# Kernel tuning notes

Measured on AMD Instinct MI355X. Metric: run time of the kernel, lower is better.

The kernel has to match this reference:

```python
import jax, jax.numpy as jnp
import numpy as np


def setup_inputs() -> dict:
    key = jax.random.key(0)
    k1, k2, k3 = jax.random.split(key, 3)
    B, N, D = 4, 256, 128
    s = jax.random.normal(k1, (B, N, D), dtype=jnp.float32)
    W1 = jax.random.normal(k2, (3 * D, 2 * D), dtype=jnp.float32) * 0.02
    b1 = jnp.zeros((2 * D,), dtype=jnp.float32)
    W2 = jax.random.normal(k3, (2 * D, 1), dtype=jnp.float32) * 0.02
    b2 = jnp.zeros((1,), dtype=jnp.float32)
    return {"s": s, "W1": W1, "b1": b1, "W2": W2, "b2": b2, "K": 8}


def reference(s, W1, b1, W2, b2, K):
    B, N, D = s.shape
    si = jnp.broadcast_to(s[:, :, None, :], (B, N, N, D))
    sj = jnp.broadcast_to(s[:, None, :, :], (B, N, N, D))
    pair = jnp.concatenate([si, sj, si * sj], axis=-1)  # [B,N,N,3D]
    h = jax.nn.relu(pair @ W1 + b1)                      # [B,N,N,2D]
    scores = (h @ W2 + b2)[..., 0]                       # [B,N,N]
    k = min(int(K), N)
    _, idx = jax.lax.top_k(scores, k)                    # [B,N,K]
    # scatter ones at topk indices (indices are distinct per row)
    gate = jnp.sum(jax.nn.one_hot(idx, N, dtype=jnp.float32), axis=-2)  # [B,N,N]
    w = gate / jnp.clip(jnp.sum(gate, axis=-1, keepdims=True), 1.0)
    ctx = jnp.einsum('bij,bjd->bid', w, s)               # [B,N,D]
    return ctx, gate, w
```

## Files before the change

kernel.cpp:

```cpp
#include <hip/hip_runtime.h>
#include <hip/hip_bf16.h>
#include <math.h>

#define B_ 4
#define N_ 256
#define D_ 128
#define H_ 256
#define K_ 8

typedef __attribute__((ext_vector_type(8))) short short8;
typedef __attribute__((ext_vector_type(4))) float f32x4;

__device__ __forceinline__ unsigned short f2bf(float x) {
    union { __hip_bfloat16 h; unsigned short s; } u;
    u.h = __float2bfloat16(x);
    return u.s;
}
__device__ __forceinline__ float bf2f(unsigned short b) {
    unsigned v = ((unsigned)b) << 16;
    return __builtin_bit_cast(float, v);
}
__device__ __forceinline__ unsigned pk2(float x, float y) {
    union { __hip_bfloat162 h; unsigned u; } c;
    c.h = __float22bfloat162_rn(float2{x, y});
    return c.u;
}
__device__ __forceinline__ void gld_lds16(const float* g, float* l) {
    __builtin_amdgcn_global_load_lds(
        (const __attribute__((address_space(1))) void*)g,
        (__attribute__((address_space(3))) void*)l, 16, 0, 0);
}

__global__ __launch_bounds__(256) void pre_kernel(
    const float* __restrict__ s, const float* __restrict__ W1,
    const float* __restrict__ b1,
    float* __restrict__ avec, float* __restrict__ bvec,
    unsigned short* __restrict__ Wt)
{
    int blk = blockIdx.x;
    int t = threadIdx.x;
    if (blk < 512) {
        int bi0 = blk * 2;
        __shared__ float s2[2][D_];
        {
            int r = t >> 7, d = t & 127;
            s2[r][d] = s[(size_t)(bi0 + r) * D_ + d];
        }
        __syncthreads();
        float aA0 = b1[t], aA1 = aA0, aB0 = 0.f, aB1 = 0.f;
        const float* W1a = W1 + t;
        const float* W1b = W1 + (size_t)D_ * H_ + t;
        #pragma unroll 8
        for (int d = 0; d < D_; ++d) {
            float wa = W1a[(size_t)d * H_];
            float wb = W1b[(size_t)d * H_];
            float s0 = s2[0][d], s1 = s2[1][d];
            aA0 = fmaf(s0, wa, aA0);
            aA1 = fmaf(s1, wa, aA1);
            aB0 = fmaf(s0, wb, aB0);
            aB1 = fmaf(s1, wb, aB1);
        }
        avec[(size_t)bi0 * H_ + t]       = aA0;
        avec[(size_t)(bi0 + 1) * H_ + t] = aA1;
        bvec[(size_t)bi0 * H_ + t]       = aB0;
        bvec[(size_t)(bi0 + 1) * H_ + t] = aB1;
    } else {
        int e = (blk - 512) * 256 + t;
        int h = e >> 7, d = e & 127;
        Wt[e] = f2bf(W1[(size_t)(2 * D_ + d) * H_ + h]);
    }
}

__global__ __launch_bounds__(512, 2) void approx_scores(
    const float* __restrict__ s, const unsigned short* __restrict__ Wt,
    const float* __restrict__ W2, const float* __restrict__ b2,
    const float* __restrict__ avec, const float* __restrict__ bvec,
    unsigned short* __restrict__ ascu)
{
    int blk = blockIdx.x;
    int b   = blk >> 7;
    int jtb = ((blk >> 4) & 7) * 32;
    int i0  = (blk & 15) * 16;
    int t = threadIdx.x;
    int lane = t & 63;
    int w = __builtin_amdgcn_readfirstlane(t >> 6);
    int l15 = lane & 15, quad = lane >> 4;

    __shared__ __align__(16) short Pl[2][32 * 128];
    __shared__ __align__(16) float si_all[16][D_];
    __shared__ __align__(16) float av_l[16][H_];
    __shared__ float partial[2][8][32];

    const float* sB = s + (size_t)b * N_ * D_;

    {
        const float* avp = avec + (size_t)(b * N_ + i0) * H_;
        #pragma unroll
        for (int k = 0; k < 2; ++k) {
            int slot = t + 512 * k;
            gld_lds16(avp + slot * 4, &av_l[0][0] + slot * 4);
        }
    }

    {
        int ii = t >> 5, dq = t & 31;
        *(float4*)&si_all[ii][dq * 4] =
            *(const float4*)(sB + (size_t)(i0 + ii) * D_ + dq * 4);
    }

    short8 Wreg[2][4];
    #pragma unroll
    for (int mi = 0; mi < 2; ++mi)
        #pragma unroll
        for (int dk = 0; dk < 4; ++dk)
            Wreg[mi][dk] = *(const short8*)(
                Wt + (size_t)(w * 32 + mi * 16 + l15) * D_ + dk * 32 + quad * 8);
    float bvr[2][2][4];
    float w2r[2][4];
    #pragma unroll
    for (int mi = 0; mi < 2; ++mi) {
        int hq = w * 32 + mi * 16 + quad * 4;
        #pragma unroll
        for (int r = 0; r < 4; ++r)
            w2r[mi][r] = W2[hq + r];
        #pragma unroll
        for (int nj = 0; nj < 2; ++nj)
            #pragma unroll
            for (int r = 0; r < 4; ++r)
                bvr[mi][nj][r] = bvec[((size_t)(b * N_ + jtb + nj * 16 + l15)) * H_
                                      + hq + r];
    }
    float b2v = b2[0];

    int prow = t >> 4, pseg = t & 15;
    float4 sj0, sj1;
    {
        const float* sj = sB + (size_t)(jtb + prow) * D_ + pseg * 8;
        sj0 = ((const float4*)sj)[0];
        sj1 = ((const float4*)sj)[1];
    }
    __syncthreads();

    {
        const float* si = &si_all[0][pseg * 8];
        float4 s0 = ((const float4*)si)[0], s1 = ((const float4*)si)[1];
        uint4 v;
        v.x = pk2(sj0.x * s0.x, sj0.y * s0.y);
        v.y = pk2(sj0.z * s0.z, sj0.w * s0.w);
        v.z = pk2(sj1.x * s1.x, sj1.y * s1.y);
        v.w = pk2(sj1.z * s1.z, sj1.w * s1.w);
        int pc = pseg ^ (prow & 15);
        *(uint4*)&Pl[0][prow * 128 + pc * 8] = v;
    }
    __syncthreads();

    #pragma unroll 1
    for (int i = 0; i < 16; ++i) {
        int cur = i & 1;
        if (w == 0 && lane < 32 && i > 0) {
            float sum = b2v;
            #pragma unroll
            for (int ww = 0; ww < 8; ++ww) sum += partial[(i - 1) & 1][ww][lane];
            ascu[(size_t)(b * N_ + i0 + i - 1) * N_ + jtb + lane] = f2bf(sum);
        }
        float4 av4[2];
        av4[0] = *(const float4*)&av_l[i][w * 32 + quad * 4];
        av4[1] = *(const float4*)&av_l[i][w * 32 + 16 + quad * 4];
        f32x4 acc[2][2];
        #pragma unroll
        for (int mi = 0; mi < 2; ++mi)
            #pragma unroll
            for (int nj = 0; nj < 2; ++nj)
                #pragma unroll
                for (int r = 0; r < 4; ++r)
                    acc[mi][nj][r] = av4[mi][r] + bvr[mi][nj][r];
        #pragma unroll
        for (int dk = 0; dk < 4; ++dk) {
            short8 Pf[2];
            #pragma unroll
            for (int nj = 0; nj < 2; ++nj) {
                int pcc = (dk * 4 + quad) ^ l15;
                Pf[nj] = *(const short8*)&Pl[cur][(nj * 16 + l15) * 128 + pcc * 8];
            }
            #pragma unroll
            for (int nj = 0; nj < 2; ++nj)
                #pragma unroll
                for (int mi = 0; mi < 2; ++mi)
                    acc[mi][nj] = __builtin_amdgcn_mfma_f32_16x16x32_bf16(
                        Wreg[mi][dk], Pf[nj], acc[mi][nj], 0, 0, 0);
        }
        if (i < 15) {
            const float* si = &si_all[i + 1][pseg * 8];
            float4 s0 = ((const float4*)si)[0], s1 = ((const float4*)si)[1];
            uint4 v;
            v.x = pk2(sj0.x * s0.x, sj0.y * s0.y);
            v.y = pk2(sj0.z * s0.z, sj0.w * s0.w);
            v.z = pk2(sj1.x * s1.x, sj1.y * s1.y);
            v.w = pk2(sj1.z * s1.z, sj1.w * s1.w);
            int pc = pseg ^ (prow & 15);
            *(uint4*)&Pl[cur ^ 1][prow * 128 + pc * 8] = v;
        }
        float rs[2];
        rs[0] = 0.f; rs[1] = 0.f;
        #pragma unroll
        for (int mi = 0; mi < 2; ++mi)
            #pragma unroll
            for (int nj = 0; nj < 2; ++nj)
                #pragma unroll
                for (int r = 0; r < 4; ++r)
                    rs[nj] = fmaf(fmaxf(acc[mi][nj][r], 0.f), w2r[mi][r], rs[nj]);
        #pragma unroll
        for (int nj = 0; nj < 2; ++nj) {
            rs[nj] += __shfl_xor(rs[nj], 16);
            rs[nj] += __shfl_xor(rs[nj], 32);
        }
        if (lane < 32) {
            float v = (quad == 0) ? rs[0] : rs[1];
            partial[cur][w][lane] = v;
        }
        __syncthreads();
    }
    if (w == 0 && lane < 32) {
        float sum = b2v;
        #pragma unroll
        for (int ww = 0; ww < 8; ++ww) sum += partial[15 & 1][ww][lane];
        ascu[(size_t)(b * N_ + i0 + 15) * N_ + jtb + lane] = f2bf(sum);
    }
}

#define DC8 8
__global__ __launch_bounds__(256) void finalize_kernel(
    const float* __restrict__ s, const float* __restrict__ W1,
    const float* __restrict__ W2, const float* __restrict__ b2,
    const float* __restrict__ avec, const float* __restrict__ bvec,
    const unsigned short* __restrict__ ascu,
    float* __restrict__ ctx, float* __restrict__ gate, float* __restrict__ w)
{
    int bi0 = blockIdx.x * 2;
    int b = bi0 >> 8;
    int t = threadIdx.x;
    int lane = t & 63;
    int wv_id = t >> 6;

    __shared__ float asc[2][N_];
    __shared__ int cand[2][16];
    __shared__ __align__(16) float Pt[D_ * 32];
    __shared__ __align__(16) float Wlw[4][2][DC8][64];
    __shared__ float part[2][16][33];
    __shared__ float rsc[2][16];
    __shared__ int sel8[2][8];

    for (int e = t; e < 512; e += 256) {
        int r = e >> 8, jj = e & 255;
        asc[r][jj] = bf2f(ascu[(size_t)(bi0 + r) * N_ + jj]);
    }
    __syncthreads();

    {
        int r = t >> 7, lj = t & 127;
        float my[2]; int rk[2];
        #pragma unroll
        for (int m = 0; m < 2; ++m) { my[m] = asc[r][m * 128 + lj]; rk[m] = 0; }
        #pragma unroll 4
        for (int j2 = 0; j2 < N_; ++j2) {
            float o = asc[r][j2];
            #pragma unroll
            for (int m = 0; m < 2; ++m) {
                int jm = m * 128 + lj;
                rk[m] += (o > my[m]) || (o == my[m] && j2 < jm);
            }
        }
        #pragma unroll
        for (int m = 0; m < 2; ++m)
            if (rk[m] < 16) cand[r][rk[m]] = m * 128 + lj;
    }
    __syncthreads();

    const float* Wc = W1 + (size_t)2 * D_ * H_;

    int dl = lane >> 4;
    int hl = (lane & 15) * 4;

    #pragma unroll
    for (int k = 0; k < 2; ++k)
        gld_lds16(Wc + (size_t)(k * 4 + dl) * H_ + wv_id * 64 + hl,
                  &Wlw[wv_id][0][k * 4 + dl][hl]);

    for (int e = t; e < 1024; e += 256) {
        int rr = e >> 9, c = e & 15, dq = (e >> 4) & 31;
        int j = cand[rr][c];
        float4 sj = *(const float4*)(s + ((size_t)(b * N_ + j)) * D_ + dq * 4);
        float4 si = *(const float4*)(s + ((size_t)(bi0 + rr)) * D_ + dq * 4);
        int base = (dq * 4) * 32 + rr * 16 + c;
        Pt[base + 0 * 32] = si.x * sj.x;
        Pt[base + 1 * 32] = si.y * sj.y;
        Pt[base + 2 * 32] = si.z * sj.z;
        Pt[base + 3 * 32] = si.w * sj.w;
    }

    int cg = t & 3, rr = (t >> 2) & 1;
    int hg = t >> 3;
    int h0 = hg * 8;
    int ho = (hg & 7) * 8;
    float acc[4][8];
    {
        const float* av = avec + (size_t)(bi0 + rr) * H_ + h0;
        float4 av40 = *(const float4*)(av);
        float4 av41 = *(const float4*)(av + 4);
        #pragma unroll
        for (int cc = 0; cc < 4; ++cc) {
            int j = cand[rr][cg * 4 + cc];
            const float* bv = bvec + ((size_t)(b * N_ + j)) * H_ + h0;
            float4 b40 = *(const float4*)(bv);
            float4 b41 = *(const float4*)(bv + 4);
            acc[cc][0] = av40.x + b40.x;
            acc[cc][1] = av40.y + b40.y;
            acc[cc][2] = av40.z + b40.z;
            acc[cc][3] = av40.w + b40.w;
            acc[cc][4] = av41.x + b41.x;
            acc[cc][5] = av41.y + b41.y;
            acc[cc][6] = av41.z + b41.z;
            acc[cc][7] = av41.w + b41.w;
        }
    }
    __syncthreads();

    int pvoff = rr * 16 + cg * 4;
    #pragma unroll 1
    for (int ch = 0; ch < 15; ++ch) {
        int cur = ch & 1;
        {
            const float* src = Wc + (size_t)((ch + 1) * DC8) * H_;
            #pragma unroll
            for (int k = 0; k < 2; ++k)
                gld_lds16(src + (size_t)(k * 4 + dl) * H_ + wv_id * 64 + hl,
                          &Wlw[wv_id][cur ^ 1][k * 4 + dl][hl]);
        }
        asm volatile("s_waitcnt vmcnt(2)" ::: "memory");
        __builtin_amdgcn_sched_barrier(0);
        int d0 = ch * DC8;
        #pragma unroll
        for (int d = 0; d < DC8; ++d) {
            float4 pv = *(const float4*)&Pt[(d0 + d) * 32 + pvoff];
            float wvv[8];
            *(float4*)&wvv[0] = *(const float4*)&Wlw[wv_id][cur][d][ho];
            *(float4*)&wvv[4] = *(const float4*)&Wlw[wv_id][cur][d][ho + 4];
            #pragma unroll
            for (int m = 0; m < 8; ++m) {
                acc[0][m] = fmaf(pv.x, wvv[m], acc[0][m]);
                acc[1][m] = fmaf(pv.y, wvv[m], acc[1][m]);
                acc[2][m] = fmaf(pv.z, wvv[m], acc[2][m]);
                acc[3][m] = fmaf(pv.w, wvv[m], acc[3][m]);
            }
        }
    }
    asm volatile("s_waitcnt vmcnt(0)" ::: "memory");
    __builtin_amdgcn_sched_barrier(0);
    {
        int d0 = 15 * DC8;
        #pragma unroll
        for (int d = 0; d < DC8; ++d) {
            float4 pv = *(const float4*)&Pt[(d0 + d) * 32 + pvoff];
            float wvv[8];
            *(float4*)&wvv[0] = *(const float4*)&Wlw[wv_id][1][d][ho];
            *(float4*)&wvv[4] = *(const float4*)&Wlw[wv_id][1][d][ho + 4];
            #pragma unroll
            for (int m = 0; m < 8; ++m) {
                acc[0][m] = fmaf(pv.x, wvv[m], acc[0][m]);
                acc[1][m] = fmaf(pv.y, wvv[m], acc[1][m]);
                acc[2][m] = fmaf(pv.z, wvv[m], acc[2][m]);
                acc[3][m] = fmaf(pv.w, wvv[m], acc[3][m]);
            }
        }
    }

    {
        float w2v[8];
        *(float4*)&w2v[0] = *(const float4*)(W2 + h0);
        *(float4*)&w2v[4] = *(const float4*)(W2 + h0 + 4);
        #pragma unroll
        for (int cc = 0; cc < 4; ++cc) {
            float sc = 0.f;
            #pragma unroll
            for (int m = 0; m < 8; ++m)
                sc = fmaf(fmaxf(acc[cc][m], 0.f), w2v[m], sc);
            part[rr][cg * 4 + cc][hg] = sc;
        }
    }
    __syncthreads();
    if (t < 32) {
        int r2 = t >> 4, c2 = t & 15;
        float sum = b2[0];
        #pragma unroll
        for (int m = 0; m < 32; ++m) sum += part[r2][c2][m];
        rsc[r2][c2] = sum;
    }
    __syncthreads();

    if (t < 32) {
        int r2 = t >> 4, c2 = t & 15;
        float my = rsc[r2][c2]; int myj = cand[r2][c2];
        int rank = 0;
        #pragma unroll
        for (int c3 = 0; c3 < 16; ++c3) {
            float o = rsc[r2][c3]; int oj = cand[r2][c3];
            rank += (o > my) || (o == my && oj < myj);
        }
        if (rank < 8) sel8[r2][rank] = myj;
    }
    __syncthreads();

    for (int e = t; e < 512; e += 256) {
        int r2 = e >> 8, jj = e & 255;
        float gv = 0.f;
        #pragma unroll
        for (int m = 0; m < 8; ++m)
            gv = (jj == sel8[r2][m]) ? 1.f : gv;
        gate[(size_t)(bi0 + r2) * N_ + jj] = gv;
        w[(size_t)(bi0 + r2) * N_ + jj]    = gv * 0.125f;
    }
    {
        int r2 = t >> 7, d = t & 127;
        float a = 0.f;
        #pragma unroll
        for (int m = 0; m < 8; ++m)
            a += s[((size_t)(b * N_ + sel8[r2][m])) * D_ + d];
        ctx[(size_t)(bi0 + r2) * D_ + d] = a * 0.125f;
    }
}

extern "C" void kernel_launch(void* const* d_in, const int* in_sizes, int n_in,
                              void* d_out, int out_size, void* d_ws, size_t ws_size,
                              hipStream_t stream)
{
    const float* s  = (const float*)d_in[0];
    const float* W1 = (const float*)d_in[1];
    const float* b1 = (const float*)d_in[2];
    const float* W2 = (const float*)d_in[3];
    const float* b2 = (const float*)d_in[4];

    float* avec = (float*)d_ws;
    float* bvec = avec + (size_t)B_ * N_ * H_;
    unsigned short* ascu = (unsigned short*)(bvec + (size_t)B_ * N_ * H_);
    unsigned short* Wtu  = ascu + (size_t)B_ * N_ * N_;

    float* ctx  = (float*)d_out;
    float* gate = ctx + (size_t)B_ * N_ * D_;
    float* wout = gate + (size_t)B_ * N_ * N_;

    pre_kernel<<<640, 256, 0, stream>>>(s, W1, b1, avec, bvec, Wtu);
    approx_scores<<<512, 512, 0, stream>>>(s, Wtu, W2, b2, avec, bvec, ascu);
    finalize_kernel<<<B_ * N_ / 2, 256, 0, stream>>>(s, W1, W2, b2, avec, bvec, ascu,
                                                     ctx, gate, wout);
}
```

Measured before the change: 128.6 us.

## Retile approx_scores to 8 i-rows by 64 j-columns and raise occupancy hint

Changes the approx_scores block tile from 16 i × 32 j to 8 i × 64 j, doubling MFMA N-tiles per wave and halving the serial i-loop length. The bvec bias is no longer kept in registers; it is reloaded from global each iteration and added after the MFMA together with avec. The launch bound goes from 2 to 4 waves per EU to allow more resident blocks. The aim is shorter per-block latency and better latency hiding, at the cost of repeated bvec global loads and more register pressure under the tighter bound.

```diff
diff --git a/kernel.cpp b/kernel.cpp
--- a/kernel.cpp
+++ b/kernel.cpp
@@ -71,7 +71,7 @@
     }
 }
 
-__global__ __launch_bounds__(512, 2) void approx_scores(
+__global__ __launch_bounds__(512, 4) void approx_scores(
     const float* __restrict__ s, const unsigned short* __restrict__ Wt,
     const float* __restrict__ W2, const float* __restrict__ b2,
     const float* __restrict__ avec, const float* __restrict__ bvec,
@@ -79,30 +79,26 @@
 {
     int blk = blockIdx.x;
     int b   = blk >> 7;
-    int jtb = ((blk >> 4) & 7) * 32;
-    int i0  = (blk & 15) * 16;
+    int jtb = ((blk >> 5) & 3) * 64;
+    int i0  = (blk & 31) * 8;
     int t = threadIdx.x;
     int lane = t & 63;
     int w = __builtin_amdgcn_readfirstlane(t >> 6);
     int l15 = lane & 15, quad = lane >> 4;
 
-    __shared__ __align__(16) short Pl[2][32 * 128];
-    __shared__ __align__(16) float si_all[16][D_];
-    __shared__ __align__(16) float av_l[16][H_];
-    __shared__ float partial[2][8][32];
+    __shared__ __align__(16) short Pl[2][64 * 128];
+    __shared__ __align__(16) float si_all[8][D_];
+    __shared__ __align__(16) float av_l[8][H_];
+    __shared__ float partial[2][8][64];
 
     const float* sB = s + (size_t)b * N_ * D_;
 
     {
         const float* avp = avec + (size_t)(b * N_ + i0) * H_;
-        #pragma unroll
-        for (int k = 0; k < 2; ++k) {
-            int slot = t + 512 * k;
-            gld_lds16(avp + slot * 4, &av_l[0][0] + slot * 4);
-        }
-    }
-
-    {
+        gld_lds16(avp + t * 4, &av_l[0][0] + t * 4);
+    }
+
+    if (t < 256) {
         int ii = t >> 5, dq = t & 31;
         *(float4*)&si_all[ii][dq * 4] =
             *(const float4*)(sB + (size_t)(i0 + ii) * D_ + dq * 4);
@@ -115,7 +111,6 @@
         for (int dk = 0; dk < 4; ++dk)
             Wreg[mi][dk] = *(const short8*)(
                 Wt + (size_t)(w * 32 + mi * 16 + l15) * D_ + dk * 32 + quad * 8);
-    float bvr[2][2][4];
     float w2r[2][4];
     #pragma unroll
     for (int mi = 0; mi < 2; ++mi) {
@@ -123,108 +118,126 @@
         #pragma unroll
         for (int r = 0; r < 4; ++r)
             w2r[mi][r] = W2[hq + r];
-        #pragma unroll
-        for (int nj = 0; nj < 2; ++nj)
-            #pragma unroll
-            for (int r = 0; r < 4; ++r)
-                bvr[mi][nj][r] = bvec[((size_t)(b * N_ + jtb + nj * 16 + l15)) * H_
-                                      + hq + r];
     }
     float b2v = b2[0];
 
     int prow = t >> 4, pseg = t & 15;
-    float4 sj0, sj1;
-    {
-        const float* sj = sB + (size_t)(jtb + prow) * D_ + pseg * 8;
-        sj0 = ((const float4*)sj)[0];
-        sj1 = ((const float4*)sj)[1];
+    float4 sjA0, sjA1, sjB0, sjB1;
+    {
+        const float* sjA = sB + (size_t)(jtb + prow) * D_ + pseg * 8;
+        sjA0 = ((const float4*)sjA)[0];
+        sjA1 = ((const float4*)sjA)[1];
+        const float* sjB = sB + (size_t)(jtb + prow + 32) * D_ + pseg * 8;
+        sjB0 = ((const float4*)sjB)[0];
+        sjB1 = ((const float4*)sjB)[1];
     }
     __syncthreads();
 
     {
         const float* si = &si_all[0][pseg * 8];
         float4 s0 = ((const float4*)si)[0], s1 = ((const float4*)si)[1];
+        int pc = pseg ^ (prow & 15);
         uint4 v;
-        v.x = pk2(sj0.x * s0.x, sj0.y * s0.y);
-        v.y = pk2(sj0.z * s0.z, sj0.w * s0.w);
-        v.z = pk2(sj1.x * s1.x, sj1.y * s1.y);
-        v.w = pk2(sj1.z * s1.z, sj1.w * s1.w);
-        int pc = pseg ^ (prow & 15);
+        v.x = pk2(sjA0.x * s0.x, sjA0.y * s0.y);
+        v.y = pk2(sjA0.z * s0.z, sjA0.w * s0.w);
+        v.z = pk2(sjA1.x * s1.x, sjA1.y * s1.y);
+        v.w = pk2(sjA1.z * s1.z, sjA1.w * s1.w);
         *(uint4*)&Pl[0][prow * 128 + pc * 8] = v;
+        uint4 u;
+        u.x = pk2(sjB0.x * s0.x, sjB0.y * s0.y);
+        u.y = pk2(sjB0.z * s0.z, sjB0.w * s0.w);
+        u.z = pk2(sjB1.x * s1.x, sjB1.y * s1.y);
+        u.w = pk2(sjB1.z * s1.z, sjB1.w * s1.w);
+        *(uint4*)&Pl[0][(prow + 32) * 128 + pc * 8] = u;
     }
     __syncthreads();
 
     #pragma unroll 1
-    for (int i = 0; i < 16; ++i) {
+    for (int i = 0; i < 8; ++i) {
         int cur = i & 1;
-        if (w == 0 && lane < 32 && i > 0) {
+        if (w == 0 && i > 0) {
             float sum = b2v;
             #pragma unroll
             for (int ww = 0; ww < 8; ++ww) sum += partial[(i - 1) & 1][ww][lane];
             ascu[(size_t)(b * N_ + i0 + i - 1) * N_ + jtb + lane] = f2bf(sum);
         }
-        float4 av4[2];
-        av4[0] = *(const float4*)&av_l[i][w * 32 + quad * 4];
-        av4[1] = *(const float4*)&av_l[i][w * 32 + 16 + quad * 4];
-        f32x4 acc[2][2];
+        float4 bv4[2][4];
         #pragma unroll
         for (int mi = 0; mi < 2; ++mi)
             #pragma unroll
-            for (int nj = 0; nj < 2; ++nj)
-                #pragma unroll
-                for (int r = 0; r < 4; ++r)
-                    acc[mi][nj][r] = av4[mi][r] + bvr[mi][nj][r];
+            for (int nj = 0; nj < 4; ++nj)
+                bv4[mi][nj] = *(const float4*)&bvec[
+                    ((size_t)(b * N_ + jtb + nj * 16 + l15)) * H_
+                    + w * 32 + mi * 16 + quad * 4];
+        f32x4 acc[2][4];
+        #pragma unroll
+        for (int mi = 0; mi < 2; ++mi)
+            #pragma unroll
+            for (int nj = 0; nj < 4; ++nj)
+                acc[mi][nj] = (f32x4){0.f, 0.f, 0.f, 0.f};
         #pragma unroll
         for (int dk = 0; dk < 4; ++dk) {
-            short8 Pf[2];
-            #pragma unroll
-            for (int nj = 0; nj < 2; ++nj) {
-                int pcc = (dk * 4 + quad) ^ l15;
+            short8 Pf[4];
+            int pcc = (dk * 4 + quad) ^ l15;
+            #pragma unroll
+            for (int nj = 0; nj < 4; ++nj)
                 Pf[nj] = *(const short8*)&Pl[cur][(nj * 16 + l15) * 128 + pcc * 8];
-            }
-            #pragma unroll
-            for (int nj = 0; nj < 2; ++nj)
+            #pragma unroll
+            for (int nj = 0; nj < 4; ++nj)
                 #pragma unroll
                 for (int mi = 0; mi < 2; ++mi)
                     acc[mi][nj] = __builtin_amdgcn_mfma_f32_16x16x32_bf16(
                         Wreg[mi][dk], Pf[nj], acc[mi][nj], 0, 0, 0);
         }
-        if (i < 15) {
+        if (i < 7) {
             const float* si = &si_all[i + 1][pseg * 8];
             float4 s0 = ((const float4*)si)[0], s1 = ((const float4*)si)[1];
+            int pc = pseg ^ (prow & 15);
             uint4 v;
-            v.x = pk2(sj0.x * s0.x, sj0.y * s0.y);
-            v.y = pk2(sj0.z * s0.z, sj0.w * s0.w);
-            v.z = pk2(sj1.x * s1.x, sj1.y * s1.y);
-            v.w = pk2(sj1.z * s1.z, sj1.w * s1.w);
-            int pc = pseg ^ (prow & 15);
+            v.x = pk2(sjA0.x * s0.x, sjA0.y * s0.y);
+            v.y = pk2(sjA0.z * s0.z, sjA0.w * s0.w);
+            v.z = pk2(sjA1.x * s1.x, sjA1.y * s1.y);
+            v.w = pk2(sjA1.z * s1.z, sjA1.w * s1.w);
             *(uint4*)&Pl[cur ^ 1][prow * 128 + pc * 8] = v;
-        }
-        float rs[2];
-        rs[0] = 0.f; rs[1] = 0.f;
+            uint4 u;
+            u.x = pk2(sjB0.x * s0.x, sjB0.y * s0.y);
+            u.y = pk2(sjB0.z * s0.z, sjB0.w * s0.w);
+            u.z = pk2(sjB1.x * s1.x, sjB1.y * s1.y);
+            u.w = pk2(sjB1.z * s1.z, sjB1.w * s1.w);
+            *(uint4*)&Pl[cur ^ 1][(prow + 32) * 128 + pc * 8] = u;
+        }
+        float4 av4[2];
+        av4[0] = *(const float4*)&av_l[i][w * 32 + quad * 4];
+        av4[1] = *(const float4*)&av_l[i][w * 32 + 16 + quad * 4];
+        float rs[4];
+        rs[0] = 0.f; rs[1] = 0.f; rs[2] = 0.f; rs[3] = 0.f;
         #pragma unroll
         for (int mi = 0; mi < 2; ++mi)
             #pragma unroll
-            for (int nj = 0; nj < 2; ++nj)
+            for (int nj = 0; nj < 4; ++nj)
                 #pragma unroll
-                for (int r = 0; r < 4; ++r)
-                    rs[nj] = fmaf(fmaxf(acc[mi][nj][r], 0.f), w2r[mi][r], rs[nj]);
-        #pragma unroll
-        for (int nj = 0; nj < 2; ++nj) {
+                for (int r = 0; r < 4; ++r) {
+                    float z = acc[mi][nj][r] + av4[mi][r] + bv4[mi][nj][r];
+                    rs[nj] = fmaf(fmaxf(z, 0.f), w2r[mi][r], rs[nj]);
+                }
+        #pragma unroll
+        for (int nj = 0; nj < 4; ++nj) {
             rs[nj] += __shfl_xor(rs[nj], 16);
             rs[nj] += __shfl_xor(rs[nj], 32);
         }
-        if (lane < 32) {
-            float v = (quad == 0) ? rs[0] : rs[1];
+        {
+            float v = (quad == 0) ? rs[0]
+                    : (quad == 1) ? rs[1]
+                    : (quad == 2) ? rs[2] : rs[3];
             partial[cur][w][lane] = v;
         }
         __syncthreads();
     }
-    if (w == 0 && lane < 32) {
+    if (w == 0) {
         float sum = b2v;
         #pragma unroll
-        for (int ww = 0; ww < 8; ++ww) sum += partial[15 & 1][ww][lane];
-        ascu[(size_t)(b * N_ + i0 + 15) * N_ + jtb + lane] = f2bf(sum);
+        for (int ww = 0; ww < 8; ++ww) sum += partial[7 & 1][ww][lane];
+        ascu[(size_t)(b * N_ + i0 + 7) * N_ + jtb + lane] = f2bf(sum);
     }
 }
 
```

Result: slower. 158.9 us (+23.5%).

## Build pair-product MFMA operands in registers and halve j-tile per block

Applied to the files above, without the earlier changes.

The approx_scores kernel now builds the si*sj bf16 B-operand directly in registers from preloaded sj rows, so the double-buffered LDS product tile and its per-iteration barrier go away. Partial sums for all 16 i rows are written to shared memory and reduced once after a single final barrier. The j-tile shrinks from 32 to 16, doubling the grid to 1024 blocks, and launch bounds allow 4 blocks per CU for more occupancy. The trade-off is that each block redoes the bf16 packing of si*sj for every i and runs fewer MFMAs per block, while holding more registers for sj.

```diff
diff --git a/kernel.cpp b/kernel.cpp
--- a/kernel.cpp
+++ b/kernel.cpp
@@ -71,25 +71,24 @@
     }
 }
 
-__global__ __launch_bounds__(512, 2) void approx_scores(
+__global__ __launch_bounds__(512, 4) void approx_scores(
     const float* __restrict__ s, const unsigned short* __restrict__ Wt,
     const float* __restrict__ W2, const float* __restrict__ b2,
     const float* __restrict__ avec, const float* __restrict__ bvec,
     unsigned short* __restrict__ ascu)
 {
     int blk = blockIdx.x;
-    int b   = blk >> 7;
-    int jtb = ((blk >> 4) & 7) * 32;
+    int b   = blk >> 8;
+    int jtb = ((blk >> 4) & 15) * 16;
     int i0  = (blk & 15) * 16;
     int t = threadIdx.x;
     int lane = t & 63;
     int w = __builtin_amdgcn_readfirstlane(t >> 6);
     int l15 = lane & 15, quad = lane >> 4;
 
-    __shared__ __align__(16) short Pl[2][32 * 128];
     __shared__ __align__(16) float si_all[16][D_];
     __shared__ __align__(16) float av_l[16][H_];
-    __shared__ float partial[2][8][32];
+    __shared__ float partial[8][16][16];
 
     const float* sB = s + (size_t)b * N_ * D_;
 
@@ -115,116 +114,71 @@
         for (int dk = 0; dk < 4; ++dk)
             Wreg[mi][dk] = *(const short8*)(
                 Wt + (size_t)(w * 32 + mi * 16 + l15) * D_ + dk * 32 + quad * 8);
-    float bvr[2][2][4];
+
+    float4 sjr[4][2];
+    {
+        const float* sj = sB + (size_t)(jtb + l15) * D_ + quad * 8;
+        #pragma unroll
+        for (int dk = 0; dk < 4; ++dk) {
+            sjr[dk][0] = ((const float4*)(sj + dk * 32))[0];
+            sjr[dk][1] = ((const float4*)(sj + dk * 32))[1];
+        }
+    }
+    float4 bvr[2];
     float w2r[2][4];
     #pragma unroll
     for (int mi = 0; mi < 2; ++mi) {
         int hq = w * 32 + mi * 16 + quad * 4;
+        bvr[mi] = *(const float4*)&bvec[((size_t)(b * N_ + jtb + l15)) * H_ + hq];
         #pragma unroll
         for (int r = 0; r < 4; ++r)
             w2r[mi][r] = W2[hq + r];
-        #pragma unroll
-        for (int nj = 0; nj < 2; ++nj)
-            #pragma unroll
-            for (int r = 0; r < 4; ++r)
-                bvr[mi][nj][r] = bvec[((size_t)(b * N_ + jtb + nj * 16 + l15)) * H_
-                                      + hq + r];
     }
     float b2v = b2[0];
-
-    int prow = t >> 4, pseg = t & 15;
-    float4 sj0, sj1;
-    {
-        const float* sj = sB + (size_t)(jtb + prow) * D_ + pseg * 8;
-        sj0 = ((const float4*)sj)[0];
-        sj1 = ((const float4*)sj)[1];
-    }
-    __syncthreads();
-
-    {
-        const float* si = &si_all[0][pseg * 8];
-        float4 s0 = ((const float4*)si)[0], s1 = ((const float4*)si)[1];
-        uint4 v;
-        v.x = pk2(sj0.x * s0.x, sj0.y * s0.y);
-        v.y = pk2(sj0.z * s0.z, sj0.w * s0.w);
-        v.z = pk2(sj1.x * s1.x, sj1.y * s1.y);
-        v.w = pk2(sj1.z * s1.z, sj1.w * s1.w);
-        int pc = pseg ^ (prow & 15);
-        *(uint4*)&Pl[0][prow * 128 + pc * 8] = v;
-    }
     __syncthreads();
 
     #pragma unroll 1
     for (int i = 0; i < 16; ++i) {
-        int cur = i & 1;
-        if (w == 0 && lane < 32 && i > 0) {
-            float sum = b2v;
-            #pragma unroll
-            for (int ww = 0; ww < 8; ++ww) sum += partial[(i - 1) & 1][ww][lane];
-            ascu[(size_t)(b * N_ + i0 + i - 1) * N_ + jtb + lane] = f2bf(sum);
-        }
-        float4 av4[2];
-        av4[0] = *(const float4*)&av_l[i][w * 32 + quad * 4];
-        av4[1] = *(const float4*)&av_l[i][w * 32 + 16 + quad * 4];
-        f32x4 acc[2][2];
+        float4 av0 = *(const float4*)&av_l[i][w * 32 + quad * 4];
+        float4 av1 = *(const float4*)&av_l[i][w * 32 + 16 + quad * 4];
+        f32x4 acc[2];
+        #pragma unroll
+        for (int r = 0; r < 4; ++r) {
+            acc[0][r] = av0[r] + bvr[0][r];
+            acc[1][r] = av1[r] + bvr[1][r];
+        }
+        #pragma unroll
+        for (int dk = 0; dk < 4; ++dk) {
+            float4 si0 = *(const float4*)&si_all[i][dk * 32 + quad * 8];
+            float4 si1 = *(const float4*)&si_all[i][dk * 32 + quad * 8 + 4];
+            union { uint4 u; short8 s8; } pf;
+            pf.u.x = pk2(sjr[dk][0].x * si0.x, sjr[dk][0].y * si0.y);
+            pf.u.y = pk2(sjr[dk][0].z * si0.z, sjr[dk][0].w * si0.w);
+            pf.u.z = pk2(sjr[dk][1].x * si1.x, sjr[dk][1].y * si1.y);
+            pf.u.w = pk2(sjr[dk][1].z * si1.z, sjr[dk][1].w * si1.w);
+            #pragma unroll
+            for (int mi = 0; mi < 2; ++mi)
+                acc[mi] = __builtin_amdgcn_mfma_f32_16x16x32_bf16(
+                    Wreg[mi][dk], pf.s8, acc[mi], 0, 0, 0);
+        }
+        float rs = 0.f;
         #pragma unroll
         for (int mi = 0; mi < 2; ++mi)
             #pragma unroll
-            for (int nj = 0; nj < 2; ++nj)
-                #pragma unroll
-                for (int r = 0; r < 4; ++r)
-                    acc[mi][nj][r] = av4[mi][r] + bvr[mi][nj][r];
-        #pragma unroll
-        for (int dk = 0; dk < 4; ++dk) {
-            short8 Pf[2];
-            #pragma unroll
-            for (int nj = 0; nj < 2; ++nj) {
-                int pcc = (dk * 4 + quad) ^ l15;
-                Pf[nj] = *(const short8*)&Pl[cur][(nj * 16 + l15) * 128 + pcc * 8];
-            }
-            #pragma unroll
-            for (int nj = 0; nj < 2; ++nj)
-                #pragma unroll
-                for (int mi = 0; mi < 2; ++mi)
-                    acc[mi][nj] = __builtin_amdgcn_mfma_f32_16x16x32_bf16(
-                        Wreg[mi][dk], Pf[nj], acc[mi][nj], 0, 0, 0);
-        }
-        if (i < 15) {
-            const float* si = &si_all[i + 1][pseg * 8];
-            float4 s0 = ((const float4*)si)[0], s1 = ((const float4*)si)[1];
-            uint4 v;
-            v.x = pk2(sj0.x * s0.x, sj0.y * s0.y);
-            v.y = pk2(sj0.z * s0.z, sj0.w * s0.w);
-            v.z = pk2(sj1.x * s1.x, sj1.y * s1.y);
-            v.w = pk2(sj1.z * s1.z, sj1.w * s1.w);
-            int pc = pseg ^ (prow & 15);
-            *(uint4*)&Pl[cur ^ 1][prow * 128 + pc * 8] = v;
-        }
-        float rs[2];
-        rs[0] = 0.f; rs[1] = 0.f;
-        #pragma unroll
-        for (int mi = 0; mi < 2; ++mi)
-            #pragma unroll
-            for (int nj = 0; nj < 2; ++nj)
-                #pragma unroll
-                for (int r = 0; r < 4; ++r)
-                    rs[nj] = fmaf(fmaxf(acc[mi][nj][r], 0.f), w2r[mi][r], rs[nj]);
-        #pragma unroll
-        for (int nj = 0; nj < 2; ++nj) {
-            rs[nj] += __shfl_xor(rs[nj], 16);
-            rs[nj] += __shfl_xor(rs[nj], 32);
-        }
-        if (lane < 32) {
-            float v = (quad == 0) ? rs[0] : rs[1];
-            partial[cur][w][lane] = v;
-        }
-        __syncthreads();
-    }
-    if (w == 0 && lane < 32) {
+            for (int r = 0; r < 4; ++r)
+                rs = fmaf(fmaxf(acc[mi][r], 0.f), w2r[mi][r], rs);
+        rs += __shfl_xor(rs, 16);
+        rs += __shfl_xor(rs, 32);
+        if (lane < 16) partial[w][i][l15] = rs;
+    }
+    __syncthreads();
+
+    if (t < 256) {
+        int i = t >> 4, j = t & 15;
         float sum = b2v;
         #pragma unroll
-        for (int ww = 0; ww < 8; ++ww) sum += partial[15 & 1][ww][lane];
-        ascu[(size_t)(b * N_ + i0 + 15) * N_ + jtb + lane] = f2bf(sum);
+        for (int ww = 0; ww < 8; ++ww) sum += partial[ww][i][j];
+        ascu[(size_t)(b * N_ + i0 + i) * N_ + jtb + j] = f2bf(sum);
     }
 }
 
@@ -449,7 +403,7 @@
     float* wout = gate + (size_t)B_ * N_ * N_;
 
     pre_kernel<<<640, 256, 0, stream>>>(s, W1, b1, avec, bvec, Wtu);
-    approx_scores<<<512, 512, 0, stream>>>(s, Wtu, W2, b2, avec, bvec, ascu);
+    approx_scores<<<1024, 512, 0, stream>>>(s, Wtu, W2, b2, avec, bvec, ascu);
     finalize_kernel<<<B_ * N_ / 2, 256, 0, stream>>>(s, W1, W2, b2, avec, bvec, ascu,
                                                      ctx, gate, wout);
 }
```

Result: slower. 142.0 us (+10.4%).
